# Kernel tuning notes

Measured on AMD Instinct MI355X. Metric: run time of the kernel, lower is better.

## Reference

```python
import jax, jax.numpy as jnp
import numpy as np

DIM = 512
N = 1024
DIM_HEAD = 64
HEADS = 8
BATCH = 8
SCALE = DIM_HEAD ** -0.5


def setup_inputs() -> dict:
    key = jax.random.key(0)
    ks = jax.random.split(key, 9)
    s = 0.02
    return {
        "x": jax.random.normal(ks[0], (BATCH, N, DIM), dtype=jnp.float32),
        "w_qkv": jax.random.normal(ks[1], (3 * DIM, DIM), dtype=jnp.float32) * s,
        "b_qkv": jax.random.normal(ks[2], (3 * DIM,), dtype=jnp.float32) * s,
        "wq": jax.random.normal(ks[3], (N, DIM_HEAD), dtype=jnp.float32) * s,
        "bq": jax.random.normal(ks[4], (N,), dtype=jnp.float32) * s,
        "wk": jax.random.normal(ks[5], (N, DIM_HEAD), dtype=jnp.float32) * s,
        "bk": jax.random.normal(ks[6], (N,), dtype=jnp.float32) * s,
        "w_out": jax.random.normal(ks[7], (DIM, DIM), dtype=jnp.float32) * s,
        "b_out": jax.random.normal(ks[8], (DIM,), dtype=jnp.float32) * s,
    }


def _split_heads(t):
    # [b, n, h*d] -> [b, h, n, d]
    b, n, _ = t.shape
    return t.reshape(b, n, HEADS, DIM_HEAD).transpose(0, 2, 1, 3)


def reference(x, w_qkv, b_qkv, wq, bq, wk, bk, w_out, b_out):
    # fused QKV projection: [b, n, 3*dim]
    qkv = x @ w_qkv.T + b_qkv
    qo, ko, vo = jnp.split(qkv, 3, axis=-1)
    q, k, v = _split_heads(qo), _split_heads(ko), _split_heads(vo)  # [b,h,n,d]

    # additive-attention stage 1: A = softmax(Wq(q) * scale) over last dim
    A = jax.nn.softmax((jnp.einsum('bhnd,md->bhnm', q, wq) + bq) * SCALE, axis=-1)  # [b,h,n,n]
    q_global = jnp.sum(jnp.einsum('bhnm,bhmd->bhnd', A, q), axis=-1, keepdims=True)  # [b,h,n,1]
    p = q_global * k  # [b,h,n,d]

    # stage 2
    B = jax.nn.softmax((jnp.einsum('bhnd,md->bhnm', p, wk) + bk) * SCALE, axis=-1)  # [b,h,n,n]
    k_global = jnp.sum(jnp.einsum('bhnm,bhmd->bhnd', B, p), axis=-1, keepdims=True)  # [b,h,n,1]

    u = (k_global * v).transpose(0, 2, 1, 3).reshape(x.shape[0], N, DIM)  # [b,n,dim]
    out = u @ w_out.T + b_out + qo
    return out
```

## Files before the change

### kernel.cpp

```cpp
#include <hip/hip_runtime.h>


#define SCL 0.125f
typedef unsigned short u16;
typedef __attribute__((ext_vector_type(8))) short short8;
typedef __attribute__((ext_vector_type(4))) float f32x4;

#define MFMA16(a, b, c) __builtin_amdgcn_mfma_f32_16x16x32_bf16((a), (b), (c), 0, 0, 0)

__device__ __forceinline__ float bf2f(u16 u) {
    union { unsigned int i; float f; } v; v.i = ((unsigned int)u) << 16; return v.f;
}
__device__ __forceinline__ u16 f2bf(float f) {
    union { float f; unsigned int i; } v; v.f = f;
    unsigned int x = v.i;
    return (u16)((x + 0x7FFFu + ((x >> 16) & 1u)) >> 16);
}

__global__ __launch_bounds__(256) void conv_kernel(
    const float* __restrict__ w_qkv, const float* __restrict__ w_out,
    const float* __restrict__ wq, const float* __restrict__ wk,
    const float* __restrict__ x, u16* __restrict__ wsb)
{
    const int idx = (blockIdx.x * 256 + threadIdx.x) * 4;
    const float* src; int off;
    if      (idx < 786432)  { src = w_qkv; off = idx; }
    else if (idx < 1048576) { src = w_out; off = idx - 786432; }
    else if (idx < 1114112) { src = wq;    off = idx - 1048576; }
    else if (idx < 1179648) { src = wk;    off = idx - 1114112; }
    else                    { src = x;     off = idx - 1179648; }
    float4 v = *(const float4*)(src + off);
    ushort4 o; o.x = f2bf(v.x); o.y = f2bf(v.y); o.z = f2bf(v.z); o.w = f2bf(v.w);
    *(ushort4*)(wsb + idx) = o;
}

#define MQK 0
#define MVU 1
#define MOUT 2

template <int MODE>
__global__ __launch_bounds__(256) void gemm_k(
    const u16* __restrict__ Ab, int lda, int acol,
    const u16* __restrict__ Wb, const float* __restrict__ bias,
    const float* __restrict__ kg, const u16* __restrict__ qkws_ro,
    u16* __restrict__ qkws, float* __restrict__ outp)
{
    __shared__ u16 As[128 * 72];
    __shared__ u16 Bs[64 * 72];
    const int t = threadIdx.x;
    const int w = t >> 6, lane = t & 63, s = lane & 15, quad = lane >> 4;
    const int bm = blockIdx.x * 128, jn0 = blockIdx.y * 64;

    f32x4 acc[2][4];
#pragma unroll
    for (int i = 0; i < 2; ++i)
#pragma unroll
        for (int j = 0; j < 4; ++j) acc[i][j] = (f32x4){0.f, 0.f, 0.f, 0.f};

    for (int kt = 0; kt < 512; kt += 64) {
        __syncthreads();
        {
            const int row = t >> 1, ch = (t & 1) * 32;
            const u16* sp = Ab + (size_t)(bm + row) * lda + acol + kt + ch;
#pragma unroll
            for (int i = 0; i < 4; ++i)
                *(uint4*)&As[row * 72 + ch + i * 8] = *(const uint4*)(sp + i * 8);
            const int r = t >> 2, bch = (t & 3) * 16;
            const u16* bp = Wb + (size_t)(jn0 + r) * 512 + kt + bch;
            *(uint4*)&Bs[r * 72 + bch]     = *(const uint4*)bp;
            *(uint4*)&Bs[r * 72 + bch + 8] = *(const uint4*)(bp + 8);
        }
        __syncthreads();
#pragma unroll
        for (int kk = 0; kk < 2; ++kk) {
            short8 a0 = *(const short8*)&As[(w * 32 + s) * 72 + kk * 32 + quad * 8];
            short8 a1 = *(const short8*)&As[(w * 32 + 16 + s) * 72 + kk * 32 + quad * 8];
#pragma unroll
            for (int ct = 0; ct < 4; ++ct) {
                short8 bf = *(const short8*)&Bs[(ct * 16 + s) * 72 + kk * 32 + quad * 8];
                acc[0][ct] = MFMA16(a0, bf, acc[0][ct]);
                acc[1][ct] = MFMA16(a1, bf, acc[1][ct]);
            }
        }
    }

    if constexpr (MODE == MOUT) {
#pragma unroll
        for (int mt = 0; mt < 2; ++mt)
#pragma unroll
            for (int ct = 0; ct < 4; ++ct) {
                const int jn = jn0 + ct * 16 + s;
#pragma unroll
                for (int r = 0; r < 4; ++r) {
                    const int row = bm + w * 32 + mt * 16 + quad * 4 + r;
                    outp[(size_t)row * 512 + jn] =
                        acc[mt][ct][r] + bias[jn] + bf2f(qkws_ro[(size_t)row * 1024 + jn]);
                }
            }
    } else {
        __syncthreads();
#pragma unroll
        for (int mt = 0; mt < 2; ++mt)
#pragma unroll
            for (int ct = 0; ct < 4; ++ct) {
                const int jn = jn0 + ct * 16 + s;
#pragma unroll
                for (int r = 0; r < 4; ++r) {
                    const int rowl = w * 32 + mt * 16 + quad * 4 + r;
                    float v = acc[mt][ct][r] + bias[jn];
                    if constexpr (MODE == MVU) {
                        const int row = bm + rowl;
                        v *= kg[(((row >> 10) * 8 + (jn >> 6)) << 10) | (row & 1023)];
                    }
                    As[rowl * 72 + ct * 16 + s] = f2bf(v);
                }
            }
        __syncthreads();
        const int row = t >> 1, ch = (t & 1) * 32;
        u16* dp = qkws + (size_t)(bm + row) * 1024 + (MODE == MVU ? 512 : 0) + jn0 + ch;
#pragma unroll
        for (int i = 0; i < 4; ++i)
            *(uint4*)(dp + i * 8) = *(const uint4*)&As[row * 72 + ch + i * 8];
    }
}

__global__ __launch_bounds__(256) void qsks_kernel(
    const u16* __restrict__ qkws, float* __restrict__ qs, float* __restrict__ ks)
{
    const int tid = blockIdx.x * 256 + threadIdx.x;
    const int n = tid & 1023, bh = tid >> 10, b = bh >> 3, h = bh & 7;
    const u16* base = qkws + (size_t)((b << 10) + n) * 1024 + (h << 6);
    float sq = 0.f, sk = 0.f;
#pragma unroll
    for (int i = 0; i < 64; i += 8) {
        union { uint4 q; u16 u[8]; } a, c;
        a.q = *(const uint4*)(base + i);
        c.q = *(const uint4*)(base + 512 + i);
#pragma unroll
        for (int j = 0; j < 8; ++j) { sq += bf2f(a.u[j]); sk += bf2f(c.u[j]); }
    }
    qs[tid] = sq; ks[tid] = sk;
}

__global__ __launch_bounds__(256) void stage_soft(
    const u16* __restrict__ qkws, int qcol0,
    const u16* __restrict__ wmb, const float* __restrict__ biasv,
    const float* __restrict__ rowscale,
    const float* __restrict__ wv1, const float* __restrict__ wv2,
    float* __restrict__ outg)
{
    __shared__ float zr[4][64], wr[4][64];
    const int t = threadIdx.x;
    const int w = t >> 6, lane = t & 63, s = lane & 15, quad = lane >> 4;
    const int n0 = blockIdx.x * 64;
    const int bh = blockIdx.y, b = bh >> 3, h = bh & 7;

    short8 qa[4][2];
#pragma unroll
    for (int nt = 0; nt < 4; ++nt)
#pragma unroll
        for (int kk = 0; kk < 2; ++kk)
            qa[nt][kk] = *(const short8*)&qkws[
                (size_t)((b << 10) + n0 + nt * 16 + s) * 1024 + qcol0 + (h << 6) + kk * 32 + quad * 8];

    float rs[4][4];
#pragma unroll
    for (int nt = 0; nt < 4; ++nt)
#pragma unroll
        for (int r = 0; r < 4; ++r)
            rs[nt][r] = rowscale ? rowscale[(bh << 10) + n0 + nt * 16 + quad * 4 + r] : 1.0f;

    float z[4][4] = {}, wa[4][4] = {};

    for (int mi = 0; mi < 16; ++mi) {
        const int mt = w * 256 + mi * 16;
        const u16* bp = wmb + (size_t)(mt + s) * 64 + quad * 8;
        short8 bf0 = *(const short8*)bp;
        short8 bf1 = *(const short8*)(bp + 32);
        const float bm = biasv[mt + s];
        float wv = wv1[(bh << 10) + mt + s];
        if (wv2) wv *= wv2[(bh << 10) + mt + s];
#pragma unroll
        for (int nt = 0; nt < 4; ++nt) {
            f32x4 a = (f32x4){0.f, 0.f, 0.f, 0.f};
            a = MFMA16(qa[nt][0], bf0, a);
            a = MFMA16(qa[nt][1], bf1, a);
#pragma unroll
            for (int r = 0; r < 4; ++r) {
                const float l = (rs[nt][r] * a[r] + bm) * SCL;
                const float e = __expf(l);
                z[nt][r] += e;
                wa[nt][r] += e * wv;
            }
        }
    }

#pragma unroll
    for (int nt = 0; nt < 4; ++nt)
#pragma unroll
        for (int r = 0; r < 4; ++r) {
            float Z = z[nt][r], W = wa[nt][r];
            for (int off = 1; off < 16; off <<= 1) {
                Z += __shfl_xor(Z, off);
                W += __shfl_xor(W, off);
            }
            if (s == 0) {
                zr[w][nt * 16 + quad * 4 + r] = Z;
                wr[w][nt * 16 + quad * 4 + r] = W;
            }
        }
    __syncthreads();
    if (t < 64) {
        float Z = zr[0][t] + zr[1][t] + zr[2][t] + zr[3][t];
        float W = wr[0][t] + wr[1][t] + wr[2][t] + wr[3][t];
        outg[(bh << 10) + n0 + t] = W / Z;
    }
}

extern "C" void kernel_launch(void* const* d_in, const int* in_sizes, int n_in,
                              void* d_out, int out_size, void* d_ws, size_t ws_size,
                              hipStream_t stream)
{
    const float* x     = (const float*)d_in[0];
    const float* w_qkv = (const float*)d_in[1];
    const float* b_qkv = (const float*)d_in[2];
    const float* wq    = (const float*)d_in[3];
    const float* bq    = (const float*)d_in[4];
    const float* wk    = (const float*)d_in[5];
    const float* bk    = (const float*)d_in[6];
    const float* w_out = (const float*)d_in[7];
    const float* b_out = (const float*)d_in[8];
    float* out = (float*)d_out;

    float* qs = (float*)d_ws;
    float* ks = qs + 65536;
    float* qg = ks + 65536;
    float* kg = qg + 65536;
    u16* wsb   = (u16*)(kg + 65536);
    u16* wqkvb = wsb;
    u16* woutb = wqkvb + 786432;
    u16* wqb   = woutb + 262144;
    u16* wkb   = wqb + 65536;
    u16* xb    = wkb + 65536;
    u16* qkws  = xb + 4194304;

    conv_kernel<<<5248, 256, 0, stream>>>(w_qkv, w_out, wq, wk, x, wsb);
    gemm_k<MQK><<<dim3(64, 16), 256, 0, stream>>>(
        xb, 512, 0, wqkvb, b_qkv, nullptr, nullptr, qkws, nullptr);
    qsks_kernel<<<256, 256, 0, stream>>>(qkws, qs, ks);
    stage_soft<<<dim3(16, 64), 256, 0, stream>>>(
        qkws, 0, wqb, bq, nullptr, qs, nullptr, qg);
    stage_soft<<<dim3(16, 64), 256, 0, stream>>>(
        qkws, 512, wkb, bk, qg, qg, ks, kg);
    gemm_k<MVU><<<dim3(64, 8), 256, 0, stream>>>(
        xb, 512, 0, wqkvb + (size_t)1024 * 512, b_qkv + 1024, kg, nullptr, qkws, nullptr);
    gemm_k<MOUT><<<dim3(64, 8), 256, 0, stream>>>(
        qkws, 1024, 512, woutb, b_out, nullptr, qkws, nullptr, out);
}
```

Before: 190.6 us.

## Fuse q/k row sums into QKV GEMM, use direct LDS loads and exp2

The QKV GEMM now computes per-head row sums of q and k in its epilogue, which removes the separate qsks kernel and the extra read of qkws it needed. GEMM tiles are staged with global_load_lds direct-to-LDS loads into unpadded shared memory, and a workgroup index swizzle is added. The QK GEMM tile widens to 128 columns. The softmax stage folds the scale and log2(e) into a single exp2 call. Unpadded LDS rows may cause bank conflicts on the fragment reads.

```diff
diff --git a/kernel.cpp b/kernel.cpp
--- a/kernel.cpp
+++ b/kernel.cpp
@@ -2,6 +2,7 @@
 
 
 #define SCL 0.125f
+#define SCL2 0.1803368801f
 typedef unsigned short u16;
 typedef __attribute__((ext_vector_type(8))) short short8;
 typedef __attribute__((ext_vector_type(4))) float f32x4;
@@ -15,6 +16,12 @@
     union { float f; unsigned int i; } v; v.f = f;
     unsigned int x = v.i;
     return (u16)((x + 0x7FFFu + ((x >> 16) & 1u)) >> 16);
+}
+
+__device__ __forceinline__ void gload16(const u16* g, u16* l) {
+    __builtin_amdgcn_global_load_lds(
+        (__attribute__((address_space(1))) void*)(void*)g,
+        (__attribute__((address_space(3))) void*)l, 16, 0, 0);
 }
 
 __global__ __launch_bounds__(256) void conv_kernel(
@@ -38,46 +45,60 @@
 #define MVU 1
 #define MOUT 2
 
-template <int MODE>
+template <int MODE, int NCT>
 __global__ __launch_bounds__(256) void gemm_k(
     const u16* __restrict__ Ab, int lda, int acol,
     const u16* __restrict__ Wb, const float* __restrict__ bias,
     const float* __restrict__ kg, const u16* __restrict__ qkws_ro,
-    u16* __restrict__ qkws, float* __restrict__ outp)
-{
-    __shared__ u16 As[128 * 72];
-    __shared__ u16 Bs[64 * 72];
+    u16* __restrict__ qkws, float* __restrict__ outp,
+    float* __restrict__ qsout, float* __restrict__ ksout)
+{
+    constexpr int BN = NCT * 16;
+    constexpr int CST = BN + 8;
+    __shared__ union SM {
+        struct { u16 A[128 * 64]; u16 B[BN * 64]; } s;
+        u16 C[128 * CST];
+    } sm;
+
     const int t = threadIdx.x;
     const int w = t >> 6, lane = t & 63, s = lane & 15, quad = lane >> 4;
-    const int bm = blockIdx.x * 128, jn0 = blockIdx.y * 64;
-
-    f32x4 acc[2][4];
+
+    const int nwgy = gridDim.y;
+    const int nwg = gridDim.x * nwgy;
+    const int flat = blockIdx.y * gridDim.x + blockIdx.x;
+    const int swz = (flat & 7) * (nwg >> 3) + (flat >> 3);
+    const int by = swz % nwgy, bx = swz / nwgy;
+    const int bm = bx * 128, jn0 = by * BN;
+
+    const int r8 = lane >> 3, c8 = (lane & 7) << 3;
+
+    f32x4 acc[2][NCT];
 #pragma unroll
     for (int i = 0; i < 2; ++i)
 #pragma unroll
-        for (int j = 0; j < 4; ++j) acc[i][j] = (f32x4){0.f, 0.f, 0.f, 0.f};
+        for (int j = 0; j < NCT; ++j) acc[i][j] = (f32x4){0.f, 0.f, 0.f, 0.f};
+
+    const u16* ga = Ab + (size_t)(bm + w * 32 + r8) * lda + acol + c8;
+    const u16* gb = Wb + (size_t)(jn0 + w * (NCT * 4) + r8) * 512 + c8;
+    u16* la = &sm.s.A[(w * 32) * 64];
+    u16* lb = &sm.s.B[(w * (NCT * 4)) * 64];
 
     for (int kt = 0; kt < 512; kt += 64) {
         __syncthreads();
-        {
-            const int row = t >> 1, ch = (t & 1) * 32;
-            const u16* sp = Ab + (size_t)(bm + row) * lda + acol + kt + ch;
-#pragma unroll
-            for (int i = 0; i < 4; ++i)
-                *(uint4*)&As[row * 72 + ch + i * 8] = *(const uint4*)(sp + i * 8);
-            const int r = t >> 2, bch = (t & 3) * 16;
-            const u16* bp = Wb + (size_t)(jn0 + r) * 512 + kt + bch;
-            *(uint4*)&Bs[r * 72 + bch]     = *(const uint4*)bp;
-            *(uint4*)&Bs[r * 72 + bch + 8] = *(const uint4*)(bp + 8);
-        }
+#pragma unroll
+        for (int j = 0; j < 4; ++j)
+            gload16(ga + (size_t)j * 8 * lda + kt, la + j * 8 * 64);
+#pragma unroll
+        for (int j = 0; j < NCT / 2; ++j)
+            gload16(gb + (size_t)j * 8 * 512 + kt, lb + j * 8 * 64);
         __syncthreads();
 #pragma unroll
         for (int kk = 0; kk < 2; ++kk) {
-            short8 a0 = *(const short8*)&As[(w * 32 + s) * 72 + kk * 32 + quad * 8];
-            short8 a1 = *(const short8*)&As[(w * 32 + 16 + s) * 72 + kk * 32 + quad * 8];
-#pragma unroll
-            for (int ct = 0; ct < 4; ++ct) {
-                short8 bf = *(const short8*)&Bs[(ct * 16 + s) * 72 + kk * 32 + quad * 8];
+            short8 a0 = *(const short8*)&sm.s.A[(w * 32 + s) * 64 + kk * 32 + quad * 8];
+            short8 a1 = *(const short8*)&sm.s.A[(w * 32 + 16 + s) * 64 + kk * 32 + quad * 8];
+#pragma unroll
+            for (int ct = 0; ct < NCT; ++ct) {
+                short8 bf = *(const short8*)&sm.s.B[(ct * 16 + s) * 64 + kk * 32 + quad * 8];
                 acc[0][ct] = MFMA16(a0, bf, acc[0][ct]);
                 acc[1][ct] = MFMA16(a1, bf, acc[1][ct]);
             }
@@ -88,7 +109,7 @@
 #pragma unroll
         for (int mt = 0; mt < 2; ++mt)
 #pragma unroll
-            for (int ct = 0; ct < 4; ++ct) {
+            for (int ct = 0; ct < NCT; ++ct) {
                 const int jn = jn0 + ct * 16 + s;
 #pragma unroll
                 for (int r = 0; r < 4; ++r) {
@@ -98,48 +119,61 @@
                 }
             }
     } else {
+        float rsum[2][NCT / 4][4];
+        if constexpr (MODE == MQK) {
+#pragma unroll
+            for (int mt = 0; mt < 2; ++mt)
+#pragma unroll
+                for (int hg = 0; hg < NCT / 4; ++hg)
+#pragma unroll
+                    for (int r = 0; r < 4; ++r) rsum[mt][hg][r] = 0.f;
+        }
         __syncthreads();
 #pragma unroll
         for (int mt = 0; mt < 2; ++mt)
 #pragma unroll
-            for (int ct = 0; ct < 4; ++ct) {
+            for (int ct = 0; ct < NCT; ++ct) {
                 const int jn = jn0 + ct * 16 + s;
+                const float bj = bias[jn];
 #pragma unroll
                 for (int r = 0; r < 4; ++r) {
                     const int rowl = w * 32 + mt * 16 + quad * 4 + r;
-                    float v = acc[mt][ct][r] + bias[jn];
+                    float v = acc[mt][ct][r] + bj;
                     if constexpr (MODE == MVU) {
                         const int row = bm + rowl;
                         v *= kg[(((row >> 10) * 8 + (jn >> 6)) << 10) | (row & 1023)];
                     }
-                    As[rowl * 72 + ct * 16 + s] = f2bf(v);
+                    if constexpr (MODE == MQK) rsum[mt][ct >> 2][r] += v;
+                    sm.C[rowl * CST + ct * 16 + s] = f2bf(v);
                 }
             }
-        __syncthreads();
-        const int row = t >> 1, ch = (t & 1) * 32;
+        if constexpr (MODE == MQK) {
+#pragma unroll
+            for (int mt = 0; mt < 2; ++mt)
+#pragma unroll
+                for (int hg = 0; hg < NCT / 4; ++hg)
+#pragma unroll
+                    for (int r = 0; r < 4; ++r) {
+                        float S = rsum[mt][hg][r];
+                        S += __shfl_xor(S, 1);
+                        S += __shfl_xor(S, 2);
+                        S += __shfl_xor(S, 4);
+                        S += __shfl_xor(S, 8);
+                        if (s == 0) {
+                            const int row = bm + w * 32 + mt * 16 + quad * 4 + r;
+                            const int jj = jn0 + hg * 64;
+                            float* dst = (jj < 512) ? qsout : ksout;
+                            dst[((((row >> 10) << 3) | ((jj >> 6) & 7)) << 10) | (row & 1023)] = S;
+                        }
+                    }
+        }
+        __syncthreads();
+        const int row = t >> 1, ch = (t & 1) * (NCT * 8);
         u16* dp = qkws + (size_t)(bm + row) * 1024 + (MODE == MVU ? 512 : 0) + jn0 + ch;
 #pragma unroll
-        for (int i = 0; i < 4; ++i)
-            *(uint4*)(dp + i * 8) = *(const uint4*)&As[row * 72 + ch + i * 8];
-    }
-}
-
-__global__ __launch_bounds__(256) void qsks_kernel(
-    const u16* __restrict__ qkws, float* __restrict__ qs, float* __restrict__ ks)
-{
-    const int tid = blockIdx.x * 256 + threadIdx.x;
-    const int n = tid & 1023, bh = tid >> 10, b = bh >> 3, h = bh & 7;
-    const u16* base = qkws + (size_t)((b << 10) + n) * 1024 + (h << 6);
-    float sq = 0.f, sk = 0.f;
-#pragma unroll
-    for (int i = 0; i < 64; i += 8) {
-        union { uint4 q; u16 u[8]; } a, c;
-        a.q = *(const uint4*)(base + i);
-        c.q = *(const uint4*)(base + 512 + i);
-#pragma unroll
-        for (int j = 0; j < 8; ++j) { sq += bf2f(a.u[j]); sk += bf2f(c.u[j]); }
-    }
-    qs[tid] = sq; ks[tid] = sk;
+        for (int i = 0; i < NCT; ++i)
+            *(uint4*)(dp + i * 8) = *(const uint4*)&sm.C[row * CST + ch + i * 8];
+    }
 }
 
 __global__ __launch_bounds__(256) void stage_soft(
@@ -163,12 +197,12 @@
             qa[nt][kk] = *(const short8*)&qkws[
                 (size_t)((b << 10) + n0 + nt * 16 + s) * 1024 + qcol0 + (h << 6) + kk * 32 + quad * 8];
 
-    float rs[4][4];
+    float rsS[4][4];
 #pragma unroll
     for (int nt = 0; nt < 4; ++nt)
 #pragma unroll
         for (int r = 0; r < 4; ++r)
-            rs[nt][r] = rowscale ? rowscale[(bh << 10) + n0 + nt * 16 + quad * 4 + r] : 1.0f;
+            rsS[nt][r] = (rowscale ? rowscale[(bh << 10) + n0 + nt * 16 + quad * 4 + r] : 1.0f) * SCL2;
 
     float z[4][4] = {}, wa[4][4] = {};
 
@@ -177,7 +211,7 @@
         const u16* bp = wmb + (size_t)(mt + s) * 64 + quad * 8;
         short8 bf0 = *(const short8*)bp;
         short8 bf1 = *(const short8*)(bp + 32);
-        const float bm = biasv[mt + s];
+        const float bm2 = biasv[mt + s] * SCL2;
         float wv = wv1[(bh << 10) + mt + s];
         if (wv2) wv *= wv2[(bh << 10) + mt + s];
 #pragma unroll
@@ -187,8 +221,7 @@
             a = MFMA16(qa[nt][1], bf1, a);
 #pragma unroll
             for (int r = 0; r < 4; ++r) {
-                const float l = (rs[nt][r] * a[r] + bm) * SCL;
-                const float e = __expf(l);
+                const float e = __builtin_amdgcn_exp2f(rsS[nt][r] * a[r] + bm2);
                 z[nt][r] += e;
                 wa[nt][r] += e * wv;
             }
@@ -245,15 +278,15 @@
     u16* qkws  = xb + 4194304;
 
     conv_kernel<<<5248, 256, 0, stream>>>(w_qkv, w_out, wq, wk, x, wsb);
-    gemm_k<MQK><<<dim3(64, 16), 256, 0, stream>>>(
-        xb, 512, 0, wqkvb, b_qkv, nullptr, nullptr, qkws, nullptr);
-    qsks_kernel<<<256, 256, 0, stream>>>(qkws, qs, ks);
+    gemm_k<MQK, 8><<<dim3(64, 8), 256, 0, stream>>>(
+        xb, 512, 0, wqkvb, b_qkv, nullptr, nullptr, qkws, nullptr, qs, ks);
     stage_soft<<<dim3(16, 64), 256, 0, stream>>>(
         qkws, 0, wqb, bq, nullptr, qs, nullptr, qg);
     stage_soft<<<dim3(16, 64), 256, 0, stream>>>(
         qkws, 512, wkb, bk, qg, qg, ks, kg);
-    gemm_k<MVU><<<dim3(64, 8), 256, 0, stream>>>(
-        xb, 512, 0, wqkvb + (size_t)1024 * 512, b_qkv + 1024, kg, nullptr, qkws, nullptr);
-    gemm_k<MOUT><<<dim3(64, 8), 256, 0, stream>>>(
-        qkws, 1024, 512, woutb, b_out, nullptr, qkws, nullptr, out);
-}
+    gemm_k<MVU, 4><<<dim3(64, 8), 256, 0, stream>>>(
+        xb, 512, 0, wqkvb + (size_t)1024 * 512, b_qkv + 1024, kg, nullptr, qkws, nullptr,
+        nullptr, nullptr);
+    gemm_k<MOUT, 4><<<dim3(64, 8), 256, 0, stream>>>(
+        qkws, 1024, 512, woutb, b_out, nullptr, qkws, nullptr, out, nullptr, nullptr);
+}
```

After: 197.7 us. 3.8% more time.
